# Kernel tuning notes

Hardware: AMD Instinct MI355X
Metric: run time of the kernel (lower is better)

The kernel has to match this reference:

```python
import jax, jax.numpy as jnp
import numpy as np

VOCAB = 90000
MAX_ID = 95000
EFFECT_DIM = 758
ADD_DIM = 10
EMBED_DIM = 768  # EFFECT_DIM + ADD_DIM
CTX = 1024
MAX_SYN = 8


def setup_inputs() -> dict:
    key = jax.random.key(0)
    k_ids, k_emb, k_rev, k_tab, k_msk = jax.random.split(key, 5)
    ids = jax.random.randint(k_ids, (CTX,), 0, VOCAB, dtype=jnp.int64)
    W_emb = jax.random.normal(k_emb, (MAX_ID, EFFECT_DIM), dtype=jnp.float32)
    W_rev = jax.random.normal(k_rev, (EMBED_DIM, MAX_ID), dtype=jnp.float32)
    padding = 0.1 * jnp.ones((CTX, ADD_DIM), dtype=jnp.float32)
    # synonym ids live in [VOCAB, MAX_ID); only some slots are active (variable-length lists)
    syn_table = jax.random.randint(k_tab, (MAX_ID, MAX_SYN), VOCAB, MAX_ID, dtype=jnp.int32)
    syn_mask = jax.random.randint(k_msk, (MAX_ID, MAX_SYN), 0, 2, dtype=jnp.int32)
    # tokens >= VOCAB (synonym ids themselves) have no synonyms
    syn_mask = syn_mask.at[VOCAB:].set(0)
    return {"ids": ids, "W_emb": W_emb, "W_rev": W_rev, "padding": padding,
            "syn_table": syn_table, "syn_mask": syn_mask}


def reference(ids, W_emb, W_rev, padding, syn_table, syn_mask):
    # VirtualEmbedding: base gather + masked synonym gather/scale/accumulate.
    # i_sum is computed BEFORE the synonym loop in the original, so each
    # synonym contribution is independent -> vectorized masked reduction.
    # (Dropout in eval mode is the identity.)
    base = W_emb[ids]                              # [L, D]
    syn_ids = syn_table[ids]                       # [L, K]
    syn = W_emb[syn_ids]                           # [L, K, D]
    mask = syn_mask[ids].astype(base.dtype)        # [L, K]
    i_sum = jnp.sum(base, axis=-1, keepdims=True)  # [L, 1]
    s_sum = jnp.sum(syn, axis=-1)                  # [L, K]
    d = i_sum / s_sum                              # [L, K]
    emb = base + jnp.einsum('lk,lkd->ld', mask * d, syn)
    # concat fixed context padding, then ReverseEmbedding projection to vocab
    full = jnp.concatenate([emb, padding], axis=1)  # [L, EMBED_DIM]
    return full @ W_rev                             # [L, MAX_ID]
```

## Files before the change

kernel.cpp:

```cpp
#include <hip/hip_runtime.h>
#include <stdint.h>

#define EFFECT_DIM 758
#define ADD_DIM 10
#define EMBED_DIM 768
#define NCOLS 95000
#define NSYN 8
#define NROWS 1024
#define NT256 372
#define TILE_B 32768

typedef __attribute__((ext_vector_type(8))) __bf16 bf16x8;
typedef __attribute__((ext_vector_type(16))) float f32x16;
typedef __attribute__((ext_vector_type(4))) uint32_t u32x4;


static __device__ __forceinline__ uint32_t pack2(float a, float b) {
  uint32_t r;
  asm("v_cvt_pk_bf16_f32 %0, %1, %2" : "=v"(r) : "v"(a), "v"(b));
  return r;
}

#define GLOAD16(src, dst)                                                   \
  __builtin_amdgcn_global_load_lds(                                         \
      (const __attribute__((address_space(1))) uint32_t*)(src),             \
      (__attribute__((address_space(3))) uint32_t*)(dst), 16, 0, 0)

__global__ __launch_bounds__(256) void emb_kernel(
    const int* __restrict__ ids, const float* __restrict__ W_emb,
    const float* __restrict__ padding, const int* __restrict__ syn_table,
    const int* __restrict__ syn_mask, char* __restrict__ ws)
{
  const int l = blockIdx.x;
  const int t = threadIdx.x;
  const int id = ids[l];
  int sid[NSYN];
  int msk[NSYN];
#pragma unroll
  for (int k = 0; k < NSYN; ++k) {
    sid[k] = syn_table[id * NSYN + k];
    msk[k] = syn_mask[id * NSYN + k];
  }

  double p[9] = {0, 0, 0, 0, 0, 0, 0, 0, 0};
  for (int d = t; d < EFFECT_DIM; d += 256) {
    p[0] += (double)W_emb[(size_t)id * EFFECT_DIM + d];
#pragma unroll
    for (int k = 0; k < NSYN; ++k)
      p[k + 1] += (double)W_emb[(size_t)sid[k] * EFFECT_DIM + d];
  }

  __shared__ double s_red[9][4];
  const int w = t >> 6;
#pragma unroll
  for (int k = 0; k < 9; ++k) {
    double v = p[k];
#pragma unroll
    for (int off = 32; off > 0; off >>= 1) v += __shfl_down(v, off, 64);
    if ((t & 63) == 0) s_red[k][w] = v;
  }
  __syncthreads();

  const double isum = s_red[0][0] + s_red[0][1] + s_red[0][2] + s_red[0][3];
  float coef[NSYN];
#pragma unroll
  for (int k = 0; k < NSYN; ++k) {
    double ss = s_red[k + 1][0] + s_red[k + 1][1] + s_red[k + 1][2] + s_red[k + 1][3];
    coef[k] = msk[k] ? (float)(isum / ss) : 0.0f;
  }

  const int r = l & 255;
  char* wbase = ws + (size_t)(l >> 8) * (12 * TILE_B);

  for (int j = t; j < 384; j += 256) {
    const int d0 = 2 * j;
    float v0, v1;
    if (d0 < EFFECT_DIM) {
      const float* bp = W_emb + (size_t)id * EFFECT_DIM + d0;
      v0 = bp[0];
      v1 = bp[1];
#pragma unroll
      for (int k = 0; k < NSYN; ++k) {
        const float* sp = W_emb + (size_t)sid[k] * EFFECT_DIM + d0;
        v0 = fmaf(coef[k], sp[0], v0);
        v1 = fmaf(coef[k], sp[1], v1);
      }
    } else {
      v0 = padding[l * ADD_DIM + (d0 - EFFECT_DIM)];
      v1 = padding[l * ADD_DIM + (d0 + 1 - EFFECT_DIM)];
    }
    const int ks   = j >> 5;
    const int jl   = j & 31;
    const int kk   = jl >> 3;
    const int byte = (jl & 7) * 4;
    const int lane = (r & 31) + ((byte >> 4) << 5);
    *(uint32_t*)(wbase + ks * TILE_B + kk * 8192 + (r >> 5) * 1024 +
                 lane * 16 + (byte & 15)) = pack2(v0, v1);
  }
}

__global__ __launch_bounds__(512, 2) void gemm_fused(
    const float* __restrict__ Wrev, const char* __restrict__ Abuf,
    float* __restrict__ out)
{
  __shared__ char lds[65536];
  const int t = threadIdx.x;
  const int l = t & 63;
  const int w = t >> 6;
  const int wm = w >> 2;
  const int wn = w & 3;

  const int wgid = blockIdx.x;
  const int xcd  = wgid & 7;
  const int work = xcd * 186 + (wgid >> 3);
  const int mt = work & 3;
  const int nt = work >> 2;
  const int n0 = nt * 256;

  const char* asrc = Abuf + (size_t)mt * (12 * TILE_B);

  const int sn = t & 255;
  const int kg = t >> 8;
  const int gn = n0 + sn;
  const bool valid = gn < NCOLS;

  float br0[16], br1[16];

#define AGLD(dst_s, s_)                                                      \
  {                                                                          \
    const char* sa = asrc + ((s_) >> 1) * TILE_B + ((s_) & 1) * 16384;       \
    GLOAD16(sa + t * 16, lds + (dst_s)*32768 + w * 1024);                    \
    GLOAD16(sa + 8192 + t * 16, lds + (dst_s)*32768 + 8192 + w * 1024);      \
  }

#define BLOAD(br, s_)                                                        \
  {                                                                          \
    const float* p = Wrev + (size_t)((s_)*32 + kg * 16) * NCOLS + gn;        \
    _Pragma("unroll") for (int j = 0; j < 16; ++j)                           \
      br[j] = valid ? p[(size_t)j * NCOLS] : 0.0f;                           \
  }

#define BSTORE(br, dst_s)                                                    \
  {                                                                          \
    _Pragma("unroll") for (int kh = 0; kh < 2; ++kh) {                       \
      u32x4 u;                                                               \
      _Pragma("unroll") for (int j = 0; j < 4; ++j)                          \
        u[j] = pack2(br[kh * 8 + 2 * j], br[kh * 8 + 2 * j + 1]);            \
      *(u32x4*)(lds + (dst_s)*32768 + 16384 + kg * 8192 + (sn >> 5) * 1024 + \
                ((sn & 31) + (kh << 5)) * 16) = u;                           \
    }                                                                        \
  }

#define COMPUTE(cs)                                                          \
  {                                                                          \
    const char* aw = lds + (cs)*32768 + (wm * 4) * 1024 + l * 16;            \
    const char* bw = lds + (cs)*32768 + 16384 + (wn * 2) * 1024 + l * 16;    \
    _Pragma("unroll") for (int p = 0; p < 2; ++p) {                          \
      bf16x8 a[4], b[2];                                                     \
      _Pragma("unroll") for (int mr = 0; mr < 4; ++mr)                       \
        a[mr] = *(const bf16x8*)(aw + p * 8192 + mr * 1024);                 \
      _Pragma("unroll") for (int nr = 0; nr < 2; ++nr)                       \
        b[nr] = *(const bf16x8*)(bw + p * 8192 + nr * 1024);                 \
      __builtin_amdgcn_s_setprio(1);                                         \
      _Pragma("unroll") for (int mr = 0; mr < 4; ++mr)                       \
        _Pragma("unroll") for (int nr = 0; nr < 2; ++nr)                     \
          acc[mr][nr] = __builtin_amdgcn_mfma_f32_32x32x16_bf16(             \
              a[mr], b[nr], acc[mr][nr], 0, 0, 0);                           \
      __builtin_amdgcn_s_setprio(0);                                         \
    }                                                                        \
  }

#define STEP(cs, SS, brCur, brNext)                                          \
  {                                                                          \
    if ((SS) + 1 < 24) AGLD((cs) ^ 1, (SS) + 1);        \
    if ((SS) + 2 < 24) BLOAD(brNext, (SS) + 2);                              \
    __builtin_amdgcn_sched_barrier(0);                                       \
    COMPUTE(cs);                                                             \
    __builtin_amdgcn_sched_barrier(0);                                       \
    if ((SS) + 1 < 24) {                                                     \
      BSTORE(brCur, (cs) ^ 1);             \
      asm volatile("s_waitcnt lgkmcnt(0)" ::: "memory");                     \
      if ((SS) + 2 < 24) asm volatile("s_waitcnt vmcnt(16)" ::: "memory");   \
      else               asm volatile("s_waitcnt vmcnt(0)" ::: "memory");    \
      __builtin_amdgcn_sched_barrier(0);                                     \
      __builtin_amdgcn_s_barrier();                                          \
    }                                                                        \
  }

  AGLD(0, 0);
  BLOAD(br0, 0);
  BSTORE(br0, 0);
  BLOAD(br0, 1);
  asm volatile("s_waitcnt lgkmcnt(0)" ::: "memory");
  __builtin_amdgcn_sched_barrier(0);
  __builtin_amdgcn_s_barrier();

  f32x16 acc[4][2] = {};

#pragma unroll
  for (int Si = 0; Si < 12; ++Si) {
    STEP(0, 2 * Si,     br0, br1);
    STEP(1, 2 * Si + 1, br1, br0);
  }
#undef STEP
#undef COMPUTE
#undef AGLD
#undef BLOAD
#undef BSTORE

  const int lh = l >> 5;
#pragma unroll
  for (int nr = 0; nr < 2; ++nr) {
    const int gc = n0 + wn * 64 + nr * 32 + (l & 31);
    if (gc < NCOLS) {
#pragma unroll
      for (int mr = 0; mr < 4; ++mr)
#pragma unroll
        for (int reg = 0; reg < 16; ++reg) {
          const int row = mt * 256 + wm * 128 + mr * 32 +
                          (reg & 3) + 8 * (reg >> 2) + 4 * lh;
          out[(size_t)row * NCOLS + gc] = acc[mr][nr][reg];
        }
    }
  }
}

extern "C" void kernel_launch(void* const* d_in, const int* in_sizes, int n_in,
                              void* d_out, int out_size, void* d_ws, size_t ws_size,
                              hipStream_t stream) {
  const int*   ids       = (const int*)d_in[0];
  const float* W_emb     = (const float*)d_in[1];
  const float* W_rev     = (const float*)d_in[2];
  const float* padding   = (const float*)d_in[3];
  const int*   syn_table = (const int*)d_in[4];
  const int*   syn_mask  = (const int*)d_in[5];
  float* out = (float*)d_out;
  char*  ws  = (char*)d_ws;

  hipLaunchKernelGGL(emb_kernel, dim3(NROWS), dim3(256), 0, stream,
                     ids, W_emb, padding, syn_table, syn_mask, ws);

  hipLaunchKernelGGL(gemm_fused, dim3(4 * NT256), dim3(512), 0, stream,
                     W_rev, ws, out);
}
```

Before: 327.0 us.

## Shrink GEMM tile to 128x128 with 256-thread blocks and simpler pipeline

The GEMM workgroup tile shrinks from 256x256 with 8 waves to 128x128 with 4 waves. LDS drops to 32KB and launch bounds allow 4 blocks per CU, with 8x743 blocks launched. The pipeline is simplified to a single B register buffer with a prefetch depth of one and a full vmcnt(0) wait each step, replacing the two-deep register double-buffer. The goal is more occupancy and finer work distribution across CUs, but each B element is now loaded once per 128-row M tile instead of once per 256, so the fp32 W_rev read traffic doubles, and the load latency is less well hidden.

```diff
diff --git a/kernel.cpp b/kernel.cpp
--- a/kernel.cpp
+++ b/kernel.cpp
@@ -7,7 +7,7 @@
 #define NCOLS 95000
 #define NSYN 8
 #define NROWS 1024
-#define NT256 372
+#define NTN 743
 #define TILE_B 32768
 
 typedef __attribute__((ext_vector_type(8))) __bf16 bf16x8;
@@ -99,70 +99,70 @@
   }
 }
 
-__global__ __launch_bounds__(512, 2) void gemm_fused(
+__global__ __launch_bounds__(256, 4) void gemm_fused(
     const float* __restrict__ Wrev, const char* __restrict__ Abuf,
     float* __restrict__ out)
 {
-  __shared__ char lds[65536];
+  __shared__ char lds[32768];
   const int t = threadIdx.x;
   const int l = t & 63;
   const int w = t >> 6;
-  const int wm = w >> 2;
-  const int wn = w & 3;
+  const int wm = w >> 1;
+  const int wn = w & 1;
 
   const int wgid = blockIdx.x;
   const int xcd  = wgid & 7;
-  const int work = xcd * 186 + (wgid >> 3);
-  const int mt = work & 3;
-  const int nt = work >> 2;
-  const int n0 = nt * 256;
-
-  const char* asrc = Abuf + (size_t)mt * (12 * TILE_B);
-
-  const int sn = t & 255;
-  const int kg = t >> 8;
-  const int gn = n0 + sn;
+  const int work = xcd * NTN + (wgid >> 3);
+  const int mt = work & 7;
+  const int nt = work >> 3;
+  const int n0 = nt * 128;
+
+  const char* asrc = Abuf + (size_t)(mt >> 1) * (12 * TILE_B) + (mt & 1) * 4096;
+
+  const int q  = t & 127;
+  const int kg = t >> 7;
+  const int gn = n0 + q;
   const bool valid = gn < NCOLS;
 
-  float br0[16], br1[16];
+  float br[16];
 
 #define AGLD(dst_s, s_)                                                      \
   {                                                                          \
     const char* sa = asrc + ((s_) >> 1) * TILE_B + ((s_) & 1) * 16384;       \
-    GLOAD16(sa + t * 16, lds + (dst_s)*32768 + w * 1024);                    \
-    GLOAD16(sa + 8192 + t * 16, lds + (dst_s)*32768 + 8192 + w * 1024);      \
-  }
-
-#define BLOAD(br, s_)                                                        \
+    GLOAD16(sa + t * 16, lds + (dst_s)*16384 + w * 1024);                    \
+    GLOAD16(sa + 8192 + t * 16, lds + (dst_s)*16384 + 4096 + w * 1024);      \
+  }
+
+#define BLOAD(s_)                                                            \
   {                                                                          \
     const float* p = Wrev + (size_t)((s_)*32 + kg * 16) * NCOLS + gn;        \
     _Pragma("unroll") for (int j = 0; j < 16; ++j)                           \
       br[j] = valid ? p[(size_t)j * NCOLS] : 0.0f;                           \
   }
 
-#define BSTORE(br, dst_s)                                                    \
+#define BSTORE(dst_s)                                                        \
   {                                                                          \
     _Pragma("unroll") for (int kh = 0; kh < 2; ++kh) {                       \
       u32x4 u;                                                               \
       _Pragma("unroll") for (int j = 0; j < 4; ++j)                          \
         u[j] = pack2(br[kh * 8 + 2 * j], br[kh * 8 + 2 * j + 1]);            \
-      *(u32x4*)(lds + (dst_s)*32768 + 16384 + kg * 8192 + (sn >> 5) * 1024 + \
-                ((sn & 31) + (kh << 5)) * 16) = u;                           \
+      *(u32x4*)(lds + (dst_s)*16384 + 8192 + kg * 4096 + (q >> 5) * 1024 +   \
+                ((q & 31) + (kh << 5)) * 16) = u;                            \
     }                                                                        \
   }
 
 #define COMPUTE(cs)                                                          \
   {                                                                          \
-    const char* aw = lds + (cs)*32768 + (wm * 4) * 1024 + l * 16;            \
-    const char* bw = lds + (cs)*32768 + 16384 + (wn * 2) * 1024 + l * 16;    \
+    const char* aw = lds + (cs)*16384 + (wm * 2) * 1024 + l * 16;            \
+    const char* bw = lds + (cs)*16384 + 8192 + (wn * 2) * 1024 + l * 16;     \
     _Pragma("unroll") for (int p = 0; p < 2; ++p) {                          \
-      bf16x8 a[4], b[2];                                                     \
-      _Pragma("unroll") for (int mr = 0; mr < 4; ++mr)                       \
-        a[mr] = *(const bf16x8*)(aw + p * 8192 + mr * 1024);                 \
+      bf16x8 a[2], b[2];                                                     \
+      _Pragma("unroll") for (int mr = 0; mr < 2; ++mr)                       \
+        a[mr] = *(const bf16x8*)(aw + p * 4096 + mr * 1024);                 \
       _Pragma("unroll") for (int nr = 0; nr < 2; ++nr)                       \
-        b[nr] = *(const bf16x8*)(bw + p * 8192 + nr * 1024);                 \
+        b[nr] = *(const bf16x8*)(bw + p * 4096 + nr * 1024);                 \
       __builtin_amdgcn_s_setprio(1);                                         \
-      _Pragma("unroll") for (int mr = 0; mr < 4; ++mr)                       \
+      _Pragma("unroll") for (int mr = 0; mr < 2; ++mr)                       \
         _Pragma("unroll") for (int nr = 0; nr < 2; ++nr)                     \
           acc[mr][nr] = __builtin_amdgcn_mfma_f32_32x32x16_bf16(             \
               a[mr], b[nr], acc[mr][nr], 0, 0, 0);                           \
@@ -170,43 +170,36 @@
     }                                                                        \
   }
 
-#define STEP(cs, SS, brCur, brNext)                                          \
-  {                                                                          \
-    if ((SS) + 1 < 24) AGLD((cs) ^ 1, (SS) + 1);        \
-    if ((SS) + 2 < 24) BLOAD(brNext, (SS) + 2);                              \
-    __builtin_amdgcn_sched_barrier(0);                                       \
-    COMPUTE(cs);                                                             \
-    __builtin_amdgcn_sched_barrier(0);                                       \
-    if ((SS) + 1 < 24) {                                                     \
-      BSTORE(brCur, (cs) ^ 1);             \
-      asm volatile("s_waitcnt lgkmcnt(0)" ::: "memory");                     \
-      if ((SS) + 2 < 24) asm volatile("s_waitcnt vmcnt(16)" ::: "memory");   \
-      else               asm volatile("s_waitcnt vmcnt(0)" ::: "memory");    \
-      __builtin_amdgcn_sched_barrier(0);                                     \
-      __builtin_amdgcn_s_barrier();                                          \
-    }                                                                        \
-  }
-
   AGLD(0, 0);
-  BLOAD(br0, 0);
-  BSTORE(br0, 0);
-  BLOAD(br0, 1);
-  asm volatile("s_waitcnt lgkmcnt(0)" ::: "memory");
-  __builtin_amdgcn_sched_barrier(0);
+  BLOAD(0);
+  BSTORE(0);
+  asm volatile("s_waitcnt vmcnt(0) lgkmcnt(0)" ::: "memory");
   __builtin_amdgcn_s_barrier();
 
-  f32x16 acc[4][2] = {};
-
-#pragma unroll
-  for (int Si = 0; Si < 12; ++Si) {
-    STEP(0, 2 * Si,     br0, br1);
-    STEP(1, 2 * Si + 1, br1, br0);
-  }
-#undef STEP
-#undef COMPUTE
+  f32x16 acc[2][2] = {};
+
+  for (int s = 0; s < 24; ++s) {
+    const int cs = s & 1;
+    const bool pf = (s < 23);
+
+    if (pf) {
+      AGLD(cs ^ 1, s + 1);
+      BLOAD(s + 1);
+    }
+    __builtin_amdgcn_sched_barrier(0);
+    COMPUTE(cs);
+    __builtin_amdgcn_sched_barrier(0);
+    if (pf) {
+      BSTORE(cs ^ 1);
+      asm volatile("s_waitcnt vmcnt(0) lgkmcnt(0)" ::: "memory");
+      __builtin_amdgcn_sched_barrier(0);
+      __builtin_amdgcn_s_barrier();
+    }
+  }
 #undef AGLD
 #undef BLOAD
 #undef BSTORE
+#undef COMPUTE
 
   const int lh = l >> 5;
 #pragma unroll
@@ -214,10 +207,10 @@
     const int gc = n0 + wn * 64 + nr * 32 + (l & 31);
     if (gc < NCOLS) {
 #pragma unroll
-      for (int mr = 0; mr < 4; ++mr)
+      for (int mr = 0; mr < 2; ++mr)
 #pragma unroll
         for (int reg = 0; reg < 16; ++reg) {
-          const int row = mt * 256 + wm * 128 + mr * 32 +
+          const int row = mt * 128 + wm * 64 + mr * 32 +
                           (reg & 3) + 8 * (reg >> 2) + 4 * lh;
           out[(size_t)row * NCOLS + gc] = acc[mr][nr][reg];
         }
@@ -240,6 +233,6 @@
   hipLaunchKernelGGL(emb_kernel, dim3(NROWS), dim3(256), 0, stream,
                      ids, W_emb, padding, syn_table, syn_mask, ws);
 
-  hipLaunchKernelGGL(gemm_fused, dim3(4 * NT256), dim3(512), 0, stream,
+  hipLaunchKernelGGL(gemm_fused, dim3(8 * NTN), dim3(256), 0, stream,
                      W_rev, ws, out);
 }
```

Result: slower. 381.1 us (+16.5%).
